# Performance work log

Measured on AMD Instinct MI355X. Metric: run time of the kernel, lower is better.

The kernel has to match this reference:

```python
import jax, jax.numpy as jnp
import numpy as np

N_NODES = 20000
N_EDGES = 500000


def setup_inputs() -> dict:
    key = jax.random.key(0)
    ks = jax.random.split(key, 12)
    s = 0.05  # small init scale for numerical sanity
    return {
        "z": jax.random.normal(ks[0], (N_NODES, 64), jnp.float32),
        "edge_index": jax.random.randint(ks[1], (2, N_EDGES), 0, N_NODES, jnp.int64),
        "celline_feats": jax.random.normal(ks[2], (N_NODES, 4), jnp.float32),
        "esm_repr": jax.random.normal(ks[3], (N_NODES, 320), jnp.float32),
        "mlp_w1": jax.random.normal(ks[4], (4, 64), jnp.float32) * s,
        "mlp_b1": jnp.zeros((64,), jnp.float32),
        "mlp_w2": jax.random.normal(ks[5], (64, 32), jnp.float32) * s,
        "mlp_b2": jnp.zeros((32,), jnp.float32),
        "mlp_w3": jax.random.normal(ks[6], (32, 16), jnp.float32) * s,
        "mlp_b3": jnp.zeros((16,), jnp.float32),
        "fc1_w": jax.random.normal(ks[7], (800, 400), jnp.float32) * s,
        "fc1_b": jnp.zeros((400,), jnp.float32),
        "fc2_w": jax.random.normal(ks[8], (400, 200), jnp.float32) * s,
        "fc2_b": jnp.zeros((200,), jnp.float32),
        "fc3_w": jax.random.normal(ks[9], (200, 100), jnp.float32) * s,
        "fc3_b": jnp.zeros((100,), jnp.float32),
        "fc4_w": jax.random.normal(ks[10], (100, 1), jnp.float32) * s,
        "fc4_b": jnp.zeros((1,), jnp.float32),
    }


def reference(z, edge_index, celline_feats, esm_repr,
              mlp_w1, mlp_b1, mlp_w2, mlp_b2, mlp_w3, mlp_b3,
              fc1_w, fc1_b, fc2_w, fc2_b, fc3_w, fc3_b, fc4_w, fc4_b):
    # cell_line_spec_mlp: 4 -> 64 -> 32 -> 16 (relu, relu, linear)
    m = jax.nn.relu(celline_feats @ mlp_w1 + mlp_b1)
    m = jax.nn.relu(m @ mlp_w2 + mlp_b2)
    m = m @ mlp_w3 + mlp_b3                       # [N, 16]
    # augment node embeddings: [N, 64+16+320] = [N, 400]
    zc = jnp.concatenate([z, m, esm_repr], axis=1)
    # gather endpoints, concat pair features: [E, 800]
    x = jnp.concatenate([zc[edge_index[0]], zc[edge_index[1]]], axis=1)
    # classifier MLP (dropout = identity in eval mode)
    x = jax.nn.relu(x @ fc1_w + fc1_b)
    x = jax.nn.relu(x @ fc2_w + fc2_b)
    x = jax.nn.relu(x @ fc3_w + fc3_b)
    x = x @ fc4_w + fc4_b                          # [E, 1]
    return jnp.squeeze(x, axis=-1)                 # [E]
```

## Files before the change

kernel.cpp:

```cpp
#include <hip/hip_runtime.h>


using u16    = unsigned short;
using f16    = _Float16;
using f16x8  = __attribute__((ext_vector_type(8))) f16;
using f32x4  = __attribute__((ext_vector_type(4))) float;
using f32x16 = __attribute__((ext_vector_type(16))) float;
using i32x4  = __attribute__((ext_vector_type(4))) int;

#define NN   20000
#define NNP  20032
#define NE   500000
#define NEP  500736
#define GRID_E 3912
#define NB   157

#define W1F_ELEMS (50*13*512)
#define W2F_ELEMS (7*26*512)
#define W3F_ELEMS (4*14*512)
#define F4_ELEMS  128
#define PREP_TOT  (W1F_ELEMS + W2F_ELEMS + W3F_ELEMS + F4_ELEMS)

#define MLP_BLOCKS  (NNP / 4)
#define PREP_BLOCKS ((PREP_TOT + 255) / 256)
#define HIST_BLOCKS ((NE + 1023) / 1024)

__device__ __forceinline__ u16 f2h(float f) {
  f16 h = (f16)f;
  return __builtin_bit_cast(u16, h);
}

__device__ __forceinline__ int cvt_pk_f16(float lo, float hi) {
  int r;
  asm("v_cvt_pkrtz_f16_f32 %0, %1, %2" : "=v"(r) : "v"(lo), "v"(hi));
  return r;
}

__device__ __forceinline__ int pk_addrelu(int p, int q) {
  int r;
  asm("v_pk_add_f16 %0, %1, %2\n\t"
      "v_pk_max_f16 %0, %0, 0"
      : "=&v"(r) : "v"(p), "v"(q));
  return r;
}

__device__ __forceinline__ void gl_lds16(const u16* g, u16* l) {
  __builtin_amdgcn_global_load_lds(
      (const __attribute__((address_space(1))) unsigned int*)g,
      (__attribute__((address_space(3))) unsigned int*)l, 16, 0, 0);
}

__global__ __launch_bounds__(256) void prep_fused(
    const float* __restrict__ cell,
    const float* __restrict__ w1, const float* __restrict__ b1,
    const float* __restrict__ w2, const float* __restrict__ b2,
    const float* __restrict__ w3, const float* __restrict__ b3,
    u16* __restrict__ mq,
    const float* __restrict__ fc1, const float* __restrict__ fc1b,
    const float* __restrict__ fc2, const float* __restrict__ fc2b,
    const float* __restrict__ fc3, const float* __restrict__ fc3b,
    const float* __restrict__ fc4,
    u16* __restrict__ W1f, u16* __restrict__ W2f, u16* __restrict__ W3f,
    float* __restrict__ fc4wp,
    const int* __restrict__ ei, int* __restrict__ hist)
{
  __shared__ float h1s[4][64];
  __shared__ float h2s[4][32];
  __shared__ int lh[NB];

  if (blockIdx.x < MLP_BLOCKS) {
    int tid = threadIdx.x, g = tid >> 6, t = tid & 63;
    int i = blockIdx.x * 4 + g;
    bool real = (i < NN);
    float c0 = 0, c1 = 0, c2 = 0, c3 = 0;
    if (real) {
      c0 = cell[(size_t)i * 4 + 0]; c1 = cell[(size_t)i * 4 + 1];
      c2 = cell[(size_t)i * 4 + 2]; c3 = cell[(size_t)i * 4 + 3];
    }
    float h = b1[t] + c0 * w1[t] + c1 * w1[64 + t] + c2 * w1[128 + t] + c3 * w1[192 + t];
    h1s[g][t] = fmaxf(h, 0.f);
    __syncthreads();
    if (t < 32) {
      float acc = b2[t];
      #pragma unroll 8
      for (int j = 0; j < 64; j++) acc += h1s[g][j] * w2[j * 32 + t];
      h2s[g][t] = fmaxf(acc, 0.f);
    }
    __syncthreads();
    if (t < 16) {
      float acc = b3[t];
      #pragma unroll 8
      for (int j = 0; j < 32; j++) acc += h2s[g][j] * w3[j * 16 + t];
      if (real) mq[(size_t)i * 16 + t] = f2h(acc);
    }
    return;
  }

  if (blockIdx.x >= MLP_BLOCKS + PREP_BLOCKS) {
    int tid = threadIdx.x;
    int base = (blockIdx.x - (MLP_BLOCKS + PREP_BLOCKS)) * 1024;
    for (int i = tid; i < NB; i += 256) lh[i] = 0;
    __syncthreads();
    #pragma unroll
    for (int k = 0; k < 4; k++) {
      int e = base + k * 256 + tid;
      if (e < NE) atomicAdd(&lh[ei[e] >> 7], 1);
    }
    __syncthreads();
    for (int i = tid; i < NB; i += 256)
      if (lh[i]) atomicAdd(&hist[i], lh[i]);
    return;
  }

  int idx = (blockIdx.x - MLP_BLOCKS) * 256 + threadIdx.x;
  if (idx < W1F_ELEMS) {
    int j = idx & 7, l = (idx >> 3) & 63, t = idx >> 9;
    int kb = t % 13, g = t / 13;
    int n = g * 16 + (l & 15);
    int k = kb * 32 + (l >> 4) * 8 + j;
    float v = 0.f;
    if (k < 400) v = (n < 400) ? fc1[(size_t)k * 400 + n]
                               : fc1[(size_t)(400 + k) * 400 + (n - 400)];
    else if (k == 400 && n < 400) v = fc1b[n];
    W1f[idx] = f2h(v);
  } else if (idx < W1F_ELEMS + W2F_ELEMS) {
    int r = idx - W1F_ELEMS;
    int j = r & 7, l = (r >> 3) & 63, t = r >> 9;
    int kb = t % 26, nt = t / 26;
    int n = nt * 32 + (l & 31);
    int k = kb * 16 + (l >> 5) * 8 + j;
    float v = 0.f;
    if (n < 200) {
      if (k < 400) v = fc2[(size_t)k * 200 + n];
      else if (k == 400) v = fc2b[n];
    }
    W2f[r] = f2h(v);
  } else if (idx < W1F_ELEMS + W2F_ELEMS + W3F_ELEMS) {
    int r = idx - (W1F_ELEMS + W2F_ELEMS);
    int j = r & 7, l = (r >> 3) & 63, t = r >> 9;
    int kb = t % 14, nt = t / 14;
    int n = nt * 32 + (l & 31);
    int k = kb * 16 + (l >> 5) * 8 + j;
    float v = 0.f;
    if (n < 100) {
      if (k < 200) v = fc3[(size_t)k * 100 + n];
      else if (k == 200) v = fc3b[n];
    }
    W3f[r] = f2h(v);
  } else if (idx < PREP_TOT) {
    int r = idx - (W1F_ELEMS + W2F_ELEMS + W3F_ELEMS);
    fc4wp[r] = (r < 100) ? fc4[r] : 0.f;
  }
}

__global__ __launch_bounds__(256) void scan_pad(
    const int* __restrict__ hist, int* __restrict__ cursor,
    int* __restrict__ sq, int* __restrict__ dq, int* __restrict__ oq)
{
  __shared__ int h[NB];
  __shared__ int cs[NB];
  int t = threadIdx.x;
  if (t < NB) h[t] = hist[t];
  __syncthreads();
  if (t == 0) {
    int run = 0;
    for (int b = 0; b < NB; b++) { cs[b] = run; run += h[b]; }
  }
  __syncthreads();
  if (t < NB) cursor[t] = cs[t];
  for (int i = NE + t; i < NEP; i += 256) {
    sq[i] = 0; dq[i] = 0; oq[i] = 0x7FFFFFFF;
  }
}

__global__ __launch_bounds__(256) void scatter_edges(
    const int* __restrict__ ei, int* __restrict__ cursor,
    int* __restrict__ sq, int* __restrict__ dq, int* __restrict__ oq)
{
  __shared__ int lh[NB];
  __shared__ int lb[NB];
  int t = threadIdx.x;
  int base = blockIdx.x * 1024;
  for (int i = t; i < NB; i += 256) lh[i] = 0;
  __syncthreads();
  int sv[4], dv[4], bv[4], rv[4];
  bool val[4];
  #pragma unroll
  for (int k = 0; k < 4; k++) {
    int e = base + k * 256 + t;
    val[k] = (e < NE);
    if (val[k]) {
      sv[k] = ei[e]; dv[k] = ei[NE + e];
      bv[k] = sv[k] >> 7;
      rv[k] = atomicAdd(&lh[bv[k]], 1);
    }
  }
  __syncthreads();
  for (int i = t; i < NB; i += 256)
    lb[i] = lh[i] ? atomicAdd(&cursor[i], lh[i]) : 0;
  __syncthreads();
  #pragma unroll
  for (int k = 0; k < 4; k++) {
    if (val[k]) {
      int pos = lb[bv[k]] + rv[k];
      sq[pos] = sv[k]; dq[pos] = dv[k]; oq[pos] = base + k * 256 + t;
    }
  }
}

#define BUILD_A(arr, row) { \
  _Pragma("unroll") \
  for (int kb = 0; kb < 13; kb++) { \
    int cst = kb * 32 + quad * 8; \
    f16x8 v; \
    if (cst < 64) { \
      const float* p = z + (size_t)(row) * 64 + cst; \
      _Pragma("unroll") for (int j = 0; j < 8; j++) v[j] = (f16)p[j]; \
    } else if (cst < 80) { \
      v = *(const f16x8*)(mq + (size_t)(row) * 16 + (cst - 64)); \
    } else if (cst < 400) { \
      const float* p = esm + (size_t)(row) * 320 + (cst - 80); \
      _Pragma("unroll") for (int j = 0; j < 8; j++) v[j] = (f16)p[j]; \
    } else { \
      _Pragma("unroll") for (int j = 0; j < 8; j++) v[j] = (f16)0.f; \
      if (cst == 400) v[0] = (f16)1.0f; \
    } \
    arr[kb] = v; \
  } }

__global__ __launch_bounds__(256) void node_gemm(
    const float* __restrict__ z, const u16* __restrict__ mq,
    const float* __restrict__ esm, const u16* __restrict__ W1f,
    u16* __restrict__ PQ)
{
  int tid = threadIdx.x, w = tid >> 6, l = tid & 63, lm = l & 15, quad = l >> 4;
  int mbase = blockIdx.x * 128 + w * 32;

  int ra = mbase + lm;       if (ra > NN - 1) ra = NN - 1;
  int rb = mbase + 16 + lm;  if (rb > NN - 1) rb = NN - 1;
  f16x8 a0[13], a1[13];
  BUILD_A(a0, ra);
  BUILD_A(a1, rb);

  for (int nt = 0; nt < 10; nt++) {
    int g = blockIdx.y * 10 + nt;
    int ncol = g * 16 + lm;
    const u16* bbase = W1f + ((size_t)g * 13 * 64 + l) * 8;
    f32x4 acc0 = {0.f, 0.f, 0.f, 0.f};
    f32x4 acc1 = {0.f, 0.f, 0.f, 0.f};
    #pragma unroll
    for (int kb = 0; kb < 13; kb++) {
      f16x8 b = *(const f16x8*)(bbase + (size_t)kb * 512);
      acc0 = __builtin_amdgcn_mfma_f32_16x16x32_f16(a0[kb], b, acc0, 0, 0, 0);
      acc1 = __builtin_amdgcn_mfma_f32_16x16x32_f16(a1[kb], b, acc1, 0, 0, 0);
    }
    #pragma unroll
    for (int r = 0; r < 4; r++) {
      int row0 = mbase + quad * 4 + r;
      int row1 = row0 + 16;
      if (row0 < NNP) PQ[(size_t)row0 * 800 + ncol] = f2h(acc0[r]);
      if (row1 < NNP) PQ[(size_t)row1 * 800 + ncol] = f2h(acc1[r]);
    }
  }
}

__global__ __launch_bounds__(256, 2) void edge_kernel(
    const u16* __restrict__ PQ, const u16* __restrict__ W2f,
    const u16* __restrict__ W3f, const float* __restrict__ fc4wp,
    const float* __restrict__ fc4b,
    const int* __restrict__ sq, const int* __restrict__ dq,
    const int* __restrict__ oq, float* __restrict__ out)
{
  __shared__ __align__(16) u16 wsm[2][26 * 512];

  int tid = threadIdx.x, w = tid >> 6, l = tid & 63;
  int c = l & 31, h = l >> 5;
  int bid = blockIdx.x;
  int idx = (bid & 7) * (GRID_E / 8) + (bid >> 3);
  int e = idx * 128 + w * 32 + c;
  int s = sq[e], d = dq[e], oi = oq[e];
  const u16* prow = PQ + (size_t)s * 800 + h * 8;
  const u16* qrow = PQ + (size_t)d * 800 + 400 + h * 8;

  for (int kb = w; kb < 26; kb += 4)
    gl_lds16(W2f + ((size_t)kb * 64 + l) * 8, &wsm[0][kb * 512]);

  i32x4 h1i[25];
  #pragma unroll
  for (int kb = 0; kb < 25; kb++) {
    i32x4 pv = *(const i32x4*)(prow + kb * 16);
    i32x4 qv = *(const i32x4*)(qrow + kb * 16);
    i32x4 r;
    #pragma unroll
    for (int j2 = 0; j2 < 4; j2++) r[j2] = pk_addrelu(pv[j2], qv[j2]);
    h1i[kb] = r;
  }
  i32x4 bias1 = {0, 0, 0, 0};
  if (h == 0) bias1[0] = 0x3C00;

  __syncthreads();

  int p2[7][8];
  #pragma unroll
  for (int nt = 0; nt < 7; nt++) {
    int cur = nt & 1;
    if (nt < 6) {
      for (int kb = w; kb < 26; kb += 4)
        gl_lds16(W2f + (((size_t)(nt + 1) * 26 + kb) * 64 + l) * 8,
                 &wsm[cur ^ 1][kb * 512]);
    } else {
      for (int kb = w; kb < 13; kb += 4)
        gl_lds16(W3f + ((size_t)kb * 64 + l) * 8, &wsm[cur ^ 1][kb * 512]);
    }
    f32x16 acc = {0.f,0.f,0.f,0.f,0.f,0.f,0.f,0.f,0.f,0.f,0.f,0.f,0.f,0.f,0.f,0.f};
    __builtin_amdgcn_s_setprio(1);
    #pragma unroll
    for (int kb = 0; kb < 25; kb++) {
      f16x8 a = *(const f16x8*)&wsm[cur][kb * 512 + l * 8];
      acc = __builtin_amdgcn_mfma_f32_32x32x16_f16(
          a, __builtin_bit_cast(f16x8, h1i[kb]), acc, 0, 0, 0);
    }
    {
      f16x8 a = *(const f16x8*)&wsm[cur][25 * 512 + l * 8];
      acc = __builtin_amdgcn_mfma_f32_32x32x16_f16(
          a, __builtin_bit_cast(f16x8, bias1), acc, 0, 0, 0);
    }
    __builtin_amdgcn_s_setprio(0);
    #pragma unroll
    for (int q = 0; q < 8; q++)
      p2[nt][q] = cvt_pk_f16(fmaxf(acc[2 * q], 0.f), fmaxf(acc[2 * q + 1], 0.f));
    __syncthreads();
  }

  i32x4 b2f[13];
  #pragma unroll
  for (int kb3 = 0; kb3 < 13; kb3++) {
    int nt = kb3 >> 1;
    i32x4 f;
    #pragma unroll
    for (int jj = 0; jj < 4; jj++) {
      int q0 = (jj & 1) + 4 * (kb3 & 1);
      if (jj < 2) {
        int x = __shfl_xor(p2[nt][q0 + 2], 32);
        f[jj] = h ? x : p2[nt][q0];
      } else {
        int y = __shfl_xor(p2[nt][q0], 32);
        f[jj] = h ? p2[nt][q0 + 2] : y;
      }
    }
    if (kb3 == 12 && h) f[0] |= 0x3C00;
    b2f[kb3] = f;
  }

  float osum = 0.f;
  #pragma unroll
  for (int nt3 = 0; nt3 < 4; nt3++) {
    int cur = (7 + nt3) & 1;
    if (nt3 < 3) {
      for (int kb = w; kb < 13; kb += 4)
        gl_lds16(W3f + (((size_t)(nt3 + 1) * 14 + kb) * 64 + l) * 8,
                 &wsm[cur ^ 1][kb * 512]);
    }
    f32x16 acc = {0.f,0.f,0.f,0.f,0.f,0.f,0.f,0.f,0.f,0.f,0.f,0.f,0.f,0.f,0.f,0.f};
    __builtin_amdgcn_s_setprio(1);
    #pragma unroll
    for (int kb3 = 0; kb3 < 13; kb3++) {
      f16x8 a = *(const f16x8*)&wsm[cur][kb3 * 512 + l * 8];
      acc = __builtin_amdgcn_mfma_f32_32x32x16_f16(
          a, __builtin_bit_cast(f16x8, b2f[kb3]), acc, 0, 0, 0);
    }
    __builtin_amdgcn_s_setprio(0);
    #pragma unroll
    for (int r = 0; r < 16; r++) {
      int rho = (r & 3) + 8 * (r >> 2) + 4 * h + 32 * nt3;
      osum += fmaxf(acc[r], 0.f) * fc4wp[rho];
    }
    if (nt3 < 3) __syncthreads();
  }
  osum += __shfl_xor(osum, 32);
  if (h == 0 && oi < NE) out[oi] = osum + fc4b[0];
}

extern "C" void kernel_launch(void* const* d_in, const int* in_sizes, int n_in,
                              void* d_out, int out_size, void* d_ws, size_t ws_size,
                              hipStream_t stream) {
  (void)in_sizes; (void)n_in; (void)out_size; (void)ws_size;
  const float* z    = (const float*)d_in[0];
  const int*   ei   = (const int*)d_in[1];
  const float* cell = (const float*)d_in[2];
  const float* esm  = (const float*)d_in[3];
  const float* w1   = (const float*)d_in[4];
  const float* b1   = (const float*)d_in[5];
  const float* w2   = (const float*)d_in[6];
  const float* b2   = (const float*)d_in[7];
  const float* w3   = (const float*)d_in[8];
  const float* b3   = (const float*)d_in[9];
  const float* fc1w = (const float*)d_in[10];
  const float* fc1b = (const float*)d_in[11];
  const float* fc2w = (const float*)d_in[12];
  const float* fc2b = (const float*)d_in[13];
  const float* fc3w = (const float*)d_in[14];
  const float* fc3b = (const float*)d_in[15];
  const float* fc4w = (const float*)d_in[16];
  const float* fc4b = (const float*)d_in[17];
  float* out = (float*)d_out;

  u16* mq  = (u16*)d_ws;
  u16* PQ  = mq  + (size_t)NNP * 16;
  u16* W1f = PQ  + (size_t)NNP * 800;
  u16* W2f = W1f + W1F_ELEMS;
  u16* W3f = W2f + W2F_ELEMS;
  float* fc4wp = (float*)(W3f + W3F_ELEMS);
  int* hist   = (int*)(fc4wp + 128);
  int* cursor = hist + 160;
  int* sq     = cursor + 160;
  int* dq     = sq + NEP;
  int* oq     = dq + NEP;

  hipMemsetAsync(hist, 0, NB * sizeof(int), stream);
  prep_fused<<<MLP_BLOCKS + PREP_BLOCKS + HIST_BLOCKS, 256, 0, stream>>>(
      cell, w1, b1, w2, b2, w3, b3, mq,
      fc1w, fc1b, fc2w, fc2b, fc3w, fc3b, fc4w, W1f, W2f, W3f, fc4wp,
      ei, hist);
  scan_pad<<<1, 256, 0, stream>>>(hist, cursor, sq, dq, oq);
  scatter_edges<<<HIST_BLOCKS, 256, 0, stream>>>(ei, cursor, sq, dq, oq);
  node_gemm<<<dim3((NNP + 127) / 128, 5), 256, 0, stream>>>(z, mq, esm, W1f, PQ);
  edge_kernel<<<GRID_E, 256, 0, stream>>>(PQ, W2f, W3f, fc4wp, fc4b,
                                          sq, dq, oq, out);
}
```

Before: 373.9 us.

## Replace global histogram scan with per-block histograms and fuse scatter into node GEMM

The histogram pass now writes per-block bucket counts instead of doing global atomics. The separate scan, scatter and node GEMM launches, plus the memset, are merged into one kernel where the scatter blocks each compute their own prefix offsets from all per-block histograms. Node GEMM A-tile loads are vectorised to float4. This cuts three launches and a single-block serial scan, at the cost of every scatter block re-reading the whole histogram table. Bucket order within a block now comes from shared-memory atomics, so edge order inside a bucket may differ from before.

```diff
diff --git a/kernel.cpp b/kernel.cpp
--- a/kernel.cpp
+++ b/kernel.cpp
@@ -24,6 +24,7 @@
 #define MLP_BLOCKS  (NNP / 4)
 #define PREP_BLOCKS ((PREP_TOT + 255) / 256)
 #define HIST_BLOCKS ((NE + 1023) / 1024)
+#define GEMM_BLOCKS (157 * 5)
 
 __device__ __forceinline__ u16 f2h(float f) {
   f16 h = (f16)f;
@@ -62,7 +63,7 @@
     const float* __restrict__ fc4,
     u16* __restrict__ W1f, u16* __restrict__ W2f, u16* __restrict__ W3f,
     float* __restrict__ fc4wp,
-    const int* __restrict__ ei, int* __restrict__ hist)
+    const int* __restrict__ ei, int* __restrict__ hist2)
 {
   __shared__ float h1s[4][64];
   __shared__ float h2s[4][32];
@@ -98,7 +99,8 @@
 
   if (blockIdx.x >= MLP_BLOCKS + PREP_BLOCKS) {
     int tid = threadIdx.x;
-    int base = (blockIdx.x - (MLP_BLOCKS + PREP_BLOCKS)) * 1024;
+    int kblk = blockIdx.x - (MLP_BLOCKS + PREP_BLOCKS);
+    int base = kblk * 1024;
     for (int i = tid; i < NB; i += 256) lh[i] = 0;
     __syncthreads();
     #pragma unroll
@@ -107,8 +109,7 @@
       if (e < NE) atomicAdd(&lh[ei[e] >> 7], 1);
     }
     __syncthreads();
-    for (int i = tid; i < NB; i += 256)
-      if (lh[i]) atomicAdd(&hist[i], lh[i]);
+    for (int i = tid; i < NB; i += 256) hist2[kblk * NB + i] = lh[i];
     return;
   }
 
@@ -153,74 +154,23 @@
   }
 }
 
-__global__ __launch_bounds__(256) void scan_pad(
-    const int* __restrict__ hist, int* __restrict__ cursor,
-    int* __restrict__ sq, int* __restrict__ dq, int* __restrict__ oq)
-{
-  __shared__ int h[NB];
-  __shared__ int cs[NB];
-  int t = threadIdx.x;
-  if (t < NB) h[t] = hist[t];
-  __syncthreads();
-  if (t == 0) {
-    int run = 0;
-    for (int b = 0; b < NB; b++) { cs[b] = run; run += h[b]; }
-  }
-  __syncthreads();
-  if (t < NB) cursor[t] = cs[t];
-  for (int i = NE + t; i < NEP; i += 256) {
-    sq[i] = 0; dq[i] = 0; oq[i] = 0x7FFFFFFF;
-  }
-}
-
-__global__ __launch_bounds__(256) void scatter_edges(
-    const int* __restrict__ ei, int* __restrict__ cursor,
-    int* __restrict__ sq, int* __restrict__ dq, int* __restrict__ oq)
-{
-  __shared__ int lh[NB];
-  __shared__ int lb[NB];
-  int t = threadIdx.x;
-  int base = blockIdx.x * 1024;
-  for (int i = t; i < NB; i += 256) lh[i] = 0;
-  __syncthreads();
-  int sv[4], dv[4], bv[4], rv[4];
-  bool val[4];
-  #pragma unroll
-  for (int k = 0; k < 4; k++) {
-    int e = base + k * 256 + t;
-    val[k] = (e < NE);
-    if (val[k]) {
-      sv[k] = ei[e]; dv[k] = ei[NE + e];
-      bv[k] = sv[k] >> 7;
-      rv[k] = atomicAdd(&lh[bv[k]], 1);
-    }
-  }
-  __syncthreads();
-  for (int i = t; i < NB; i += 256)
-    lb[i] = lh[i] ? atomicAdd(&cursor[i], lh[i]) : 0;
-  __syncthreads();
-  #pragma unroll
-  for (int k = 0; k < 4; k++) {
-    if (val[k]) {
-      int pos = lb[bv[k]] + rv[k];
-      sq[pos] = sv[k]; dq[pos] = dv[k]; oq[pos] = base + k * 256 + t;
-    }
-  }
-}
-
 #define BUILD_A(arr, row) { \
   _Pragma("unroll") \
   for (int kb = 0; kb < 13; kb++) { \
     int cst = kb * 32 + quad * 8; \
     f16x8 v; \
     if (cst < 64) { \
-      const float* p = z + (size_t)(row) * 64 + cst; \
-      _Pragma("unroll") for (int j = 0; j < 8; j++) v[j] = (f16)p[j]; \
+      const f32x4* p = (const f32x4*)(z + (size_t)(row) * 64 + cst); \
+      f32x4 u0 = p[0], u1 = p[1]; \
+      _Pragma("unroll") for (int j = 0; j < 4; j++) { \
+        v[j] = (f16)u0[j]; v[4 + j] = (f16)u1[j]; } \
     } else if (cst < 80) { \
       v = *(const f16x8*)(mq + (size_t)(row) * 16 + (cst - 64)); \
     } else if (cst < 400) { \
-      const float* p = esm + (size_t)(row) * 320 + (cst - 80); \
-      _Pragma("unroll") for (int j = 0; j < 8; j++) v[j] = (f16)p[j]; \
+      const f32x4* p = (const f32x4*)(esm + (size_t)(row) * 320 + (cst - 80)); \
+      f32x4 u0 = p[0], u1 = p[1]; \
+      _Pragma("unroll") for (int j = 0; j < 4; j++) { \
+        v[j] = (f16)u0[j]; v[4 + j] = (f16)u1[j]; } \
     } else { \
       _Pragma("unroll") for (int j = 0; j < 8; j++) v[j] = (f16)0.f; \
       if (cst == 400) v[0] = (f16)1.0f; \
@@ -228,13 +178,60 @@
     arr[kb] = v; \
   } }
 
-__global__ __launch_bounds__(256) void node_gemm(
+__global__ __launch_bounds__(256) void scatter_gemm(
     const float* __restrict__ z, const u16* __restrict__ mq,
     const float* __restrict__ esm, const u16* __restrict__ W1f,
-    u16* __restrict__ PQ)
+    u16* __restrict__ PQ,
+    const int* __restrict__ ei, const int* __restrict__ hist2,
+    int* __restrict__ sq, int* __restrict__ dq, int* __restrict__ oq)
 {
+  __shared__ int cs[NB];
+  __shared__ int pf[NB];
+  __shared__ int lh[NB];
+
+  if (blockIdx.x < HIST_BLOCKS) {
+    int k = blockIdx.x, t = threadIdx.x;
+    if (t < NB) {
+      int tot = 0, myp = 0;
+      #pragma unroll 8
+      for (int kk = 0; kk < HIST_BLOCKS; kk++) {
+        int cnt = hist2[kk * NB + t];
+        tot += cnt;
+        if (kk < k) myp += cnt;
+      }
+      cs[t] = tot;
+      pf[t] = myp;
+      lh[t] = 0;
+    }
+    __syncthreads();
+    if (t == 0) {
+      int run = 0;
+      for (int b = 0; b < NB; b++) { int v = cs[b]; cs[b] = run; run += v; }
+    }
+    __syncthreads();
+    int base = k * 1024;
+    #pragma unroll
+    for (int kk = 0; kk < 4; kk++) {
+      int e = base + kk * 256 + t;
+      if (e < NE) {
+        int s = ei[e], d = ei[NE + e];
+        int b = s >> 7;
+        int pos = cs[b] + pf[b] + atomicAdd(&lh[b], 1);
+        sq[pos] = s; dq[pos] = d; oq[pos] = e;
+      }
+    }
+    if (k == 0) {
+      for (int i = NE + t; i < NEP; i += 256) {
+        sq[i] = 0; dq[i] = 0; oq[i] = 0x7FFFFFFF;
+      }
+    }
+    return;
+  }
+
+  int bid2 = blockIdx.x - HIST_BLOCKS;
+  int bx = bid2 % 157, by = bid2 / 157;
   int tid = threadIdx.x, w = tid >> 6, l = tid & 63, lm = l & 15, quad = l >> 4;
-  int mbase = blockIdx.x * 128 + w * 32;
+  int mbase = bx * 128 + w * 32;
 
   int ra = mbase + lm;       if (ra > NN - 1) ra = NN - 1;
   int rb = mbase + 16 + lm;  if (rb > NN - 1) rb = NN - 1;
@@ -243,7 +240,7 @@
   BUILD_A(a1, rb);
 
   for (int nt = 0; nt < 10; nt++) {
-    int g = blockIdx.y * 10 + nt;
+    int g = by * 10 + nt;
     int ncol = g * 16 + lm;
     const u16* bbase = W1f + ((size_t)g * 13 * 64 + l) * 8;
     f32x4 acc0 = {0.f, 0.f, 0.f, 0.f};
@@ -411,20 +408,17 @@
   u16* W2f = W1f + W1F_ELEMS;
   u16* W3f = W2f + W2F_ELEMS;
   float* fc4wp = (float*)(W3f + W3F_ELEMS);
-  int* hist   = (int*)(fc4wp + 128);
-  int* cursor = hist + 160;
-  int* sq     = cursor + 160;
+  int* hist2  = (int*)(fc4wp + 128);
+  int* sq     = hist2 + HIST_BLOCKS * NB;
   int* dq     = sq + NEP;
   int* oq     = dq + NEP;
 
-  hipMemsetAsync(hist, 0, NB * sizeof(int), stream);
   prep_fused<<<MLP_BLOCKS + PREP_BLOCKS + HIST_BLOCKS, 256, 0, stream>>>(
       cell, w1, b1, w2, b2, w3, b3, mq,
       fc1w, fc1b, fc2w, fc2b, fc3w, fc3b, fc4w, W1f, W2f, W3f, fc4wp,
-      ei, hist);
-  scan_pad<<<1, 256, 0, stream>>>(hist, cursor, sq, dq, oq);
-  scatter_edges<<<HIST_BLOCKS, 256, 0, stream>>>(ei, cursor, sq, dq, oq);
-  node_gemm<<<dim3((NNP + 127) / 128, 5), 256, 0, stream>>>(z, mq, esm, W1f, PQ);
+      ei, hist2);
+  scatter_gemm<<<HIST_BLOCKS + GEMM_BLOCKS, 256, 0, stream>>>(
+      z, mq, esm, W1f, PQ, ei, hist2, sq, dq, oq);
   edge_kernel<<<GRID_E, 256, 0, stream>>>(PQ, W2f, W3f, fc4wp, fc4b,
                                           sq, dq, oq, out);
 }
```

Result: no change. 376.3 us (+0.6%).
